# Kernel tuning notes

Measured on AMD Instinct MI355X. Metric: run time of the kernel, lower is better.

Reference implementation:

```python
import jax, jax.numpy as jnp
import numpy as np

N, K, H = 98, 10, 4        # landmarks, neighbors/node, heads
B, CIN, HC = 1024, 256, 64 # batch, in_channels, head_channels
NEG = -9e15


def setup_inputs() -> dict:
    key = jax.random.key(0)
    ks = jax.random.split(key, 3)
    rng = np.random.default_rng(0)
    # fixed sparsity pattern: K unique neighbors per row, row-major order
    cols2d = np.stack([np.sort(rng.choice(N, K, replace=False)) for _ in range(N)])
    rows = np.repeat(np.arange(N), K)
    cols = cols2d.reshape(-1)
    x = jax.random.normal(ks[0], (B, N, CIN), jnp.float32)
    W = jax.random.normal(ks[1], (H, 2, CIN, HC), jnp.float32) * 0.05  # xavier-ish
    e = jnp.ones((H, N * K), jnp.float32)  # nn.init.constant_(e, 1)
    stdv = 1.0 / np.sqrt(HC)
    bias = jax.random.uniform(ks[2], (H, HC), jnp.float32, -stdv, stdv)
    return {"x": x, "W": W, "e": e, "bias": bias,
            "rows": jnp.asarray(rows, jnp.int32),
            "cols": jnp.asarray(cols, jnp.int32)}


def reference(x, W, e, bias, rows, cols):
    # h0/h1 for all heads at once: [2, H, B, N, HC]
    h = jnp.einsum('bnc,hscd->shbnd', x, W)
    h0, h1 = h[0], h[1]
    # masked adjacency logits per head: -9e15 everywhere, learned e at edges
    base = jnp.full((N, N), NEG, jnp.float32)
    logits = jax.vmap(lambda eh: base.at[rows, cols].set(eh))(e)  # [H,N,N]
    A = jax.nn.softmax(logits, axis=-1)  # F.softmax(adj, dim=1) on [N,N]
    diag = jnp.diagonal(A, axis1=-2, axis2=-1)  # [H,N] -> adj*M part
    A_off = A - diag[..., None] * jnp.eye(N, dtype=A.dtype)  # adj*(1-M)
    out = diag[:, None, :, None] * h0 + jnp.einsum('hij,hbjd->hbid', A_off, h1)
    out = out + bias[:, None, None, :]  # [H,B,N,HC]
    # concat heads along channel dim -> [B, N, H*HC]
    return jnp.transpose(out, (1, 2, 0, 3)).reshape(B, N, H * HC)
```

## Files before the change

kernel.cpp:

```cpp
#include <hip/hip_runtime.h>

typedef __bf16 bf16;
typedef bf16 bf16x4 __attribute__((ext_vector_type(4)));
typedef bf16 bf16x8 __attribute__((ext_vector_type(8)));
typedef float f32x4 __attribute__((ext_vector_type(4)));

#define NND 98
#define KNB 10
#define NH 4
#define CIN 256
#define HC 64
#define CROW_E 132
#define WP_BYTES 262144

__device__ __forceinline__ bf16x8 load_a8(const float* p) {
  f32x4 u = *(const f32x4*)p;
  f32x4 v = *(const f32x4*)(p + 4);
  bf16x8 a;
  a[0] = (bf16)u[0]; a[1] = (bf16)u[1]; a[2] = (bf16)u[2]; a[3] = (bf16)u[3];
  a[4] = (bf16)v[0]; a[5] = (bf16)v[1]; a[6] = (bf16)v[2]; a[7] = (bf16)v[3];
  return a;
}

__global__ __launch_bounds__(256) void prep_kernel(const float* __restrict__ W,
                                                   bf16* __restrict__ Wp,
                                                   const float* __restrict__ x,
                                                   bf16* __restrict__ xa, int B) {
  if (blockIdx.x < 64) {
    int t = blockIdx.x * 256 + threadIdx.x;
    if (t >= 8 * 8 * 4 * 64) return;
    int lane = t & 63;
    int nt = (t >> 6) & 3;
    int kt = (t >> 8) & 7;
    int hs = t >> 11;
    int n = nt * 16 + (lane & 15);
    int kb = kt * 32 + (lane >> 4) * 8;
    const float* src = W + (hs * CIN + kb) * HC + n;
    bf16x8 v;
#pragma unroll
    for (int j = 0; j < 8; ++j) v[j] = (bf16)src[j * HC];
    *(bf16x8*)(Wp + (long long)t * 8) = v;
    return;
  }
  int u = (blockIdx.x - 64) * 256 + threadIdx.x;
  int total = B * 7 * 8 * 64;
  if (u >= total) return;
  int lane = u & 63;
  int kt = (u >> 6) & 7;
  int v = u >> 9;
  int b = v / 7;
  int mt = v - b * 7;
  int row = mt * 16 + (lane & 15);
  int k0 = kt * 32 + (lane >> 4) * 8;
  bf16x8 a = {};
  if (row < NND) a = load_a8(x + ((long long)b * NND + row) * CIN + k0);
  *(bf16x8*)(xa + (long long)u * 8) = a;
}

template <bool XA>
__global__ __launch_bounds__(512, 4) void semgconv_kernel(
    const float* __restrict__ x, const bf16* __restrict__ xa,
    const float* __restrict__ e, const float* __restrict__ bias,
    const int* __restrict__ cols, const bf16* __restrict__ Wp,
    float* __restrict__ out, int nwg) {
  __shared__ __align__(16) bf16 C[112 * CROW_E];
  __shared__ float w_lds[NND * KNB];
  __shared__ short cols_lds[NND * KNB];
  __shared__ float diag_lds[NND];

  const int tid = threadIdx.x;
  int n = blockIdx.x;
  int w = ((nwg & 7) == 0) ? ((n & 7) * (nwg >> 3) + (n >> 3)) : n;
  const int b = w >> 2;
  const int h = w & 3;

  const int lane = tid & 63;
  const int wv = tid >> 6;
  const int wm = wv & 3;
  const int sh = wv >> 2;
  const int mt0 = wm * 2;
  const bool has1 = (mt0 + 1 < 7);

  if (tid < NND) {
    const int i = tid;
    const int* cp = cols + i * KNB;
    const float* ep = e + (h * NND + i) * KNB;
    float ev[KNB];
    int cv[KNB];
    float mx = -3.0e38f;
#pragma unroll
    for (int j = 0; j < KNB; ++j) { cv[j] = cp[j]; ev[j] = ep[j]; mx = fmaxf(mx, ev[j]); }
    float s = 0.f;
#pragma unroll
    for (int j = 0; j < KNB; ++j) { ev[j] = __expf(ev[j] - mx); s += ev[j]; }
    const float inv = 1.f / s;
    float dg = 0.f;
#pragma unroll
    for (int j = 0; j < KNB; ++j) {
      float wj = ev[j] * inv;
      if (cv[j] == i) { dg = wj; wj = 0.f; }
      w_lds[i * KNB + j] = wj;
      cols_lds[i * KNB + j] = (short)cv[j];
    }
    diag_lds[i] = dg;
  }

  f32x4 acc[2][4] = {};
  {
    const bf16* wpl = Wp + ((long long)((h * 2 + sh) * 32) * 64 + lane) * 8;
    if (XA) {
      const bf16* ax0 = xa + (((long long)b * 7 + mt0) * 8 * 64 + lane) * 8;
      const bf16* ax1 = ax0 + 8 * 64 * 8;
#pragma unroll
      for (int kt = 0; kt < 8; ++kt) {
        bf16x8 afr0 = *(const bf16x8*)(ax0 + kt * 512);
        bf16x8 afr1 = {};
        if (has1) afr1 = *(const bf16x8*)(ax1 + kt * 512);
        bf16x8 bfr[4];
#pragma unroll
        for (int nt = 0; nt < 4; ++nt)
          bfr[nt] = *(const bf16x8*)(wpl + (long long)((kt * 4 + nt) * 64) * 8);
#pragma unroll
        for (int nt = 0; nt < 4; ++nt)
          acc[0][nt] = __builtin_amdgcn_mfma_f32_16x16x32_bf16(afr0, bfr[nt], acc[0][nt], 0, 0, 0);
        if (has1) {
#pragma unroll
          for (int nt = 0; nt < 4; ++nt)
            acc[1][nt] = __builtin_amdgcn_mfma_f32_16x16x32_bf16(afr1, bfr[nt], acc[1][nt], 0, 0, 0);
        }
      }
    } else {
      const float* xb = x + (long long)b * (NND * CIN);
      const int r0 = mt0 * 16 + (lane & 15);
      const int kb = (lane >> 4) * 8;
      const float* ap0 = xb + r0 * CIN + kb;
      const float* ap1 = ap0 + 16 * CIN;
      const bool ok0 = (r0 < NND);
#pragma unroll
      for (int kt = 0; kt < 8; ++kt) {
        bf16x8 afr0 = {}, afr1 = {};
        if (ok0) afr0 = load_a8(ap0 + kt * 32);
        if (has1) afr1 = load_a8(ap1 + kt * 32);
        bf16x8 bfr[4];
#pragma unroll
        for (int nt = 0; nt < 4; ++nt)
          bfr[nt] = *(const bf16x8*)(wpl + (long long)((kt * 4 + nt) * 64) * 8);
#pragma unroll
        for (int nt = 0; nt < 4; ++nt)
          acc[0][nt] = __builtin_amdgcn_mfma_f32_16x16x32_bf16(afr0, bfr[nt], acc[0][nt], 0, 0, 0);
        if (has1) {
#pragma unroll
          for (int nt = 0; nt < 4; ++nt)
            acc[1][nt] = __builtin_amdgcn_mfma_f32_16x16x32_bf16(afr1, bfr[nt], acc[1][nt], 0, 0, 0);
        }
      }
    }
  }

  {
    const int rowb = mt0 * 16 + (lane >> 4) * 4;
    const int colb = sh * 64 + (lane & 15);
#pragma unroll
    for (int im = 0; im < 2; ++im) {
      if (mt0 + im < 7) {
#pragma unroll
        for (int nt = 0; nt < 4; ++nt) {
          const int col = colb + nt * 16;
#pragma unroll
          for (int r = 0; r < 4; ++r)
            C[(rowb + im * 16 + r) * CROW_E + col] = (bf16)acc[im][nt][r];
        }
      }
    }
  }
  __syncthreads();

  {
    const int d4 = (tid & 15) * 4;
    const int ig = tid >> 4;
    f32x4 bs = *(const f32x4*)(bias + h * HC + d4);
    float* outb = out + (long long)b * (NND * NH * HC) + h * HC + d4;
#pragma unroll
    for (int p = 0; p < 4; ++p) {
      const int i = p * 32 + ig;
      if (i < NND) {
        f32x4 av = bs;
        const float dg = diag_lds[i];
        bf16x4 c0 = *(const bf16x4*)(C + i * CROW_E + d4);
        av[0] += dg * (float)c0[0];
        av[1] += dg * (float)c0[1];
        av[2] += dg * (float)c0[2];
        av[3] += dg * (float)c0[3];
#pragma unroll
        for (int j = 0; j < KNB; ++j) {
          const float wj = w_lds[i * KNB + j];
          const int cj = cols_lds[i * KNB + j];
          bf16x4 c1 = *(const bf16x4*)(C + cj * CROW_E + HC + d4);
          av[0] += wj * (float)c1[0];
          av[1] += wj * (float)c1[1];
          av[2] += wj * (float)c1[2];
          av[3] += wj * (float)c1[3];
        }
        *(f32x4*)(outb + (long long)i * (NH * HC)) = av;
      }
    }
  }
}

extern "C" void kernel_launch(void* const* d_in, const int* in_sizes, int n_in,
                              void* d_out, int out_size, void* d_ws, size_t ws_size,
                              hipStream_t stream) {
  const float* x    = (const float*)d_in[0];
  const float* W    = (const float*)d_in[1];
  const float* e    = (const float*)d_in[2];
  const float* bias = (const float*)d_in[3];
  const int* cols   = (const int*)d_in[5];
  float* out        = (float*)d_out;

  int B = in_sizes[0] / (NND * CIN);

  bf16* Wp = (bf16*)d_ws;
  bf16* xa = (bf16*)((char*)d_ws + WP_BYTES);
  const long long xa_bytes = (long long)B * 7 * 8 * 64 * 8 * (long long)sizeof(bf16);
  const bool use_xa = (long long)ws_size >= (long long)WP_BYTES + xa_bytes;

  int xa_blocks = use_xa ? (B * 7 * 8 * 64) / 256 : 0;
  prep_kernel<<<64 + xa_blocks, 256, 0, stream>>>(W, Wp, x, xa, B);

  const int nwg = B * NH;
  if (use_xa)
    semgconv_kernel<true><<<nwg, 512, 0, stream>>>(x, xa, e, bias, cols, Wp, out, nwg);
  else
    semgconv_kernel<false><<<nwg, 512, 0, stream>>>(x, xa, e, bias, cols, Wp, out, nwg);
}
```

Measured before the change: 245.4 us.

## Process two batch elements per workgroup to reuse W fragments and softmax setup

Each workgroup now handles two batch items for one head, loading each W fragment once and feeding it into MFMAs for both items, and doubling the LDS staging buffer. The goal is to amortize W loads, the per-block edge-softmax setup and launch overhead over twice the work, halving the grid. In exchange it uses more accumulator registers and twice the LDS per block, which may lower occupancy under the 512x4 launch bound. It also assumes B is even, and an odd B would leave the last batch item unprocessed.

```diff
diff --git a/kernel.cpp b/kernel.cpp
--- a/kernel.cpp
+++ b/kernel.cpp
@@ -12,6 +12,7 @@
 #define HC 64
 #define CROW_E 132
 #define WP_BYTES 262144
+#define XA_TILE (7 * 8 * 64 * 8)
 
 __device__ __forceinline__ bf16x8 load_a8(const float* p) {
   f32x4 u = *(const f32x4*)p;
@@ -63,7 +64,7 @@
     const float* __restrict__ e, const float* __restrict__ bias,
     const int* __restrict__ cols, const bf16* __restrict__ Wp,
     float* __restrict__ out, int nwg) {
-  __shared__ __align__(16) bf16 C[112 * CROW_E];
+  __shared__ __align__(16) bf16 C2[2][112 * CROW_E];
   __shared__ float w_lds[NND * KNB];
   __shared__ short cols_lds[NND * KNB];
   __shared__ float diag_lds[NND];
@@ -71,8 +72,9 @@
   const int tid = threadIdx.x;
   int n = blockIdx.x;
   int w = ((nwg & 7) == 0) ? ((n & 7) * (nwg >> 3) + (n >> 3)) : n;
-  const int b = w >> 2;
+  const int bp = w >> 2;
   const int h = w & 3;
+  const int b0 = bp * 2;
 
   const int lane = tid & 63;
   const int wv = tid >> 6;
@@ -105,54 +107,64 @@
     diag_lds[i] = dg;
   }
 
-  f32x4 acc[2][4] = {};
+  f32x4 acc[2][2][4] = {};
   {
     const bf16* wpl = Wp + ((long long)((h * 2 + sh) * 32) * 64 + lane) * 8;
     if (XA) {
-      const bf16* ax0 = xa + (((long long)b * 7 + mt0) * 8 * 64 + lane) * 8;
-      const bf16* ax1 = ax0 + 8 * 64 * 8;
+      const bf16* ax0 = xa + (((long long)b0 * 7 + mt0) * 8 * 64 + lane) * 8;
+      const bf16* ax1 = ax0 + XA_TILE;
 #pragma unroll
       for (int kt = 0; kt < 8; ++kt) {
-        bf16x8 afr0 = *(const bf16x8*)(ax0 + kt * 512);
-        bf16x8 afr1 = {};
-        if (has1) afr1 = *(const bf16x8*)(ax1 + kt * 512);
+        bf16x8 a00 = *(const bf16x8*)(ax0 + kt * 512);
+        bf16x8 a10 = *(const bf16x8*)(ax1 + kt * 512);
+        bf16x8 a01 = {}, a11 = {};
+        if (has1) {
+          a01 = *(const bf16x8*)(ax0 + 4096 + kt * 512);
+          a11 = *(const bf16x8*)(ax1 + 4096 + kt * 512);
+        }
         bf16x8 bfr[4];
 #pragma unroll
         for (int nt = 0; nt < 4; ++nt)
           bfr[nt] = *(const bf16x8*)(wpl + (long long)((kt * 4 + nt) * 64) * 8);
 #pragma unroll
-        for (int nt = 0; nt < 4; ++nt)
-          acc[0][nt] = __builtin_amdgcn_mfma_f32_16x16x32_bf16(afr0, bfr[nt], acc[0][nt], 0, 0, 0);
+        for (int nt = 0; nt < 4; ++nt) {
+          acc[0][0][nt] = __builtin_amdgcn_mfma_f32_16x16x32_bf16(a00, bfr[nt], acc[0][0][nt], 0, 0, 0);
+          acc[1][0][nt] = __builtin_amdgcn_mfma_f32_16x16x32_bf16(a10, bfr[nt], acc[1][0][nt], 0, 0, 0);
+        }
         if (has1) {
 #pragma unroll
-          for (int nt = 0; nt < 4; ++nt)
-            acc[1][nt] = __builtin_amdgcn_mfma_f32_16x16x32_bf16(afr1, bfr[nt], acc[1][nt], 0, 0, 0);
+          for (int nt = 0; nt < 4; ++nt) {
+            acc[0][1][nt] = __builtin_amdgcn_mfma_f32_16x16x32_bf16(a01, bfr[nt], acc[0][1][nt], 0, 0, 0);
+            acc[1][1][nt] = __builtin_amdgcn_mfma_f32_16x16x32_bf16(a11, bfr[nt], acc[1][1][nt], 0, 0, 0);
+          }
         }
       }
     } else {
-      const float* xb = x + (long long)b * (NND * CIN);
       const int r0 = mt0 * 16 + (lane & 15);
       const int kb = (lane >> 4) * 8;
-      const float* ap0 = xb + r0 * CIN + kb;
-      const float* ap1 = ap0 + 16 * CIN;
       const bool ok0 = (r0 < NND);
 #pragma unroll
       for (int kt = 0; kt < 8; ++kt) {
-        bf16x8 afr0 = {}, afr1 = {};
-        if (ok0) afr0 = load_a8(ap0 + kt * 32);
-        if (has1) afr1 = load_a8(ap1 + kt * 32);
+        bf16x8 afr[2][2];
+#pragma unroll
+        for (int it2 = 0; it2 < 2; ++it2) {
+          const float* ap = x + ((long long)(b0 + it2) * NND + r0) * CIN + kb;
+          afr[it2][0] = ok0 ? load_a8(ap + kt * 32) : bf16x8{};
+          afr[it2][1] = has1 ? load_a8(ap + 16 * CIN + kt * 32) : bf16x8{};
+        }
         bf16x8 bfr[4];
 #pragma unroll
         for (int nt = 0; nt < 4; ++nt)
           bfr[nt] = *(const bf16x8*)(wpl + (long long)((kt * 4 + nt) * 64) * 8);
 #pragma unroll
-        for (int nt = 0; nt < 4; ++nt)
-          acc[0][nt] = __builtin_amdgcn_mfma_f32_16x16x32_bf16(afr0, bfr[nt], acc[0][nt], 0, 0, 0);
-        if (has1) {
-#pragma unroll
-          for (int nt = 0; nt < 4; ++nt)
-            acc[1][nt] = __builtin_amdgcn_mfma_f32_16x16x32_bf16(afr1, bfr[nt], acc[1][nt], 0, 0, 0);
-        }
+        for (int it2 = 0; it2 < 2; ++it2)
+#pragma unroll
+          for (int im = 0; im < 2; ++im)
+            if (im == 0 || has1)
+#pragma unroll
+              for (int nt = 0; nt < 4; ++nt)
+                acc[it2][im][nt] = __builtin_amdgcn_mfma_f32_16x16x32_bf16(
+                    afr[it2][im], bfr[nt], acc[it2][im][nt], 0, 0, 0);
       }
     }
   }
@@ -161,14 +173,17 @@
     const int rowb = mt0 * 16 + (lane >> 4) * 4;
     const int colb = sh * 64 + (lane & 15);
 #pragma unroll
-    for (int im = 0; im < 2; ++im) {
-      if (mt0 + im < 7) {
-#pragma unroll
-        for (int nt = 0; nt < 4; ++nt) {
-          const int col = colb + nt * 16;
-#pragma unroll
-          for (int r = 0; r < 4; ++r)
-            C[(rowb + im * 16 + r) * CROW_E + col] = (bf16)acc[im][nt][r];
+    for (int it2 = 0; it2 < 2; ++it2) {
+#pragma unroll
+      for (int im = 0; im < 2; ++im) {
+        if (mt0 + im < 7) {
+#pragma unroll
+          for (int nt = 0; nt < 4; ++nt) {
+            const int col = colb + nt * 16;
+#pragma unroll
+            for (int r = 0; r < 4; ++r)
+              C2[it2][(rowb + im * 16 + r) * CROW_E + col] = (bf16)acc[it2][im][nt][r];
+          }
         }
       }
     }
@@ -179,29 +194,33 @@
     const int d4 = (tid & 15) * 4;
     const int ig = tid >> 4;
     f32x4 bs = *(const f32x4*)(bias + h * HC + d4);
-    float* outb = out + (long long)b * (NND * NH * HC) + h * HC + d4;
-#pragma unroll
-    for (int p = 0; p < 4; ++p) {
-      const int i = p * 32 + ig;
-      if (i < NND) {
-        f32x4 av = bs;
-        const float dg = diag_lds[i];
-        bf16x4 c0 = *(const bf16x4*)(C + i * CROW_E + d4);
-        av[0] += dg * (float)c0[0];
-        av[1] += dg * (float)c0[1];
-        av[2] += dg * (float)c0[2];
-        av[3] += dg * (float)c0[3];
-#pragma unroll
-        for (int j = 0; j < KNB; ++j) {
-          const float wj = w_lds[i * KNB + j];
-          const int cj = cols_lds[i * KNB + j];
-          bf16x4 c1 = *(const bf16x4*)(C + cj * CROW_E + HC + d4);
-          av[0] += wj * (float)c1[0];
-          av[1] += wj * (float)c1[1];
-          av[2] += wj * (float)c1[2];
-          av[3] += wj * (float)c1[3];
-        }
-        *(f32x4*)(outb + (long long)i * (NH * HC)) = av;
+#pragma unroll
+    for (int it2 = 0; it2 < 2; ++it2) {
+      const bf16* C = C2[it2];
+      float* outb = out + (long long)(b0 + it2) * (NND * NH * HC) + h * HC + d4;
+#pragma unroll
+      for (int p = 0; p < 4; ++p) {
+        const int i = p * 32 + ig;
+        if (i < NND) {
+          f32x4 av = bs;
+          const float dg = diag_lds[i];
+          bf16x4 c0 = *(const bf16x4*)(C + i * CROW_E + d4);
+          av[0] += dg * (float)c0[0];
+          av[1] += dg * (float)c0[1];
+          av[2] += dg * (float)c0[2];
+          av[3] += dg * (float)c0[3];
+#pragma unroll
+          for (int j = 0; j < KNB; ++j) {
+            const float wj = w_lds[i * KNB + j];
+            const int cj = cols_lds[i * KNB + j];
+            bf16x4 c1 = *(const bf16x4*)(C + cj * CROW_E + HC + d4);
+            av[0] += wj * (float)c1[0];
+            av[1] += wj * (float)c1[1];
+            av[2] += wj * (float)c1[2];
+            av[3] += wj * (float)c1[3];
+          }
+          *(f32x4*)(outb + (long long)i * (NH * HC)) = av;
+        }
       }
     }
   }
@@ -221,13 +240,13 @@
 
   bf16* Wp = (bf16*)d_ws;
   bf16* xa = (bf16*)((char*)d_ws + WP_BYTES);
-  const long long xa_bytes = (long long)B * 7 * 8 * 64 * 8 * (long long)sizeof(bf16);
+  const long long xa_bytes = (long long)B * XA_TILE * (long long)sizeof(bf16);
   const bool use_xa = (long long)ws_size >= (long long)WP_BYTES + xa_bytes;
 
   int xa_blocks = use_xa ? (B * 7 * 8 * 64) / 256 : 0;
   prep_kernel<<<64 + xa_blocks, 256, 0, stream>>>(W, Wp, x, xa, B);
 
-  const int nwg = B * NH;
+  const int nwg = (B / 2) * NH;
   if (use_xa)
     semgconv_kernel<true><<<nwg, 512, 0, stream>>>(x, xa, e, bias, cols, Wp, out, nwg);
   else
```

Result: faster. 240.3 us (-2.0%).
